# Optimization experiments

Hardware: AMD Instinct MI355X
Metric: run time of the kernel (lower is better)

## Reference

```python
import jax, jax.numpy as jnp
import numpy as np

N = 1048576   # total nodes across batch
B = 128       # number of graphs
H = 128       # hidden_size
NEG_SLOPE = 0.01  # LeakyReLU default


def setup_inputs() -> dict:
    key = jax.random.key(0)
    k1, k2, k3, k4 = jax.random.split(key, 4)
    h = jax.random.normal(k1, (N, H), dtype=jnp.float32)
    attention_query = jax.random.normal(k2, (B, H), dtype=jnp.float32)
    w = jax.random.normal(k3, (2 * H,), dtype=jnp.float32) * (1.0 / np.sqrt(2 * H))
    segment_ids = jnp.sort(jax.random.randint(k4, (N,), 0, B, dtype=jnp.int32))
    return {"h": h, "attention_query": attention_query, "w": w, "segment_ids": segment_ids}


def reference(h, attention_query, w, segment_ids):
    # gate_nn(concat([h, q_rep])) = h @ w[:H] + q[seg] @ w[H:], then LeakyReLU
    w_h, w_q = w[:H], w[H:]
    q_score = attention_query @ w_q                      # [B]
    gate = h @ w_h + q_score[segment_ids]                # [N]
    gate = jnp.where(gate >= 0, gate, NEG_SLOPE * gate)  # LeakyReLU
    # segment softmax over nodes of each graph
    m = jax.ops.segment_max(gate, segment_ids, num_segments=B)   # [B]
    m = jnp.where(jnp.isfinite(m), m, 0.0)               # guard empty segments
    e = jnp.exp(gate - m[segment_ids])                   # [N]
    denom = jax.ops.segment_sum(e, segment_ids, num_segments=B)  # [B]
    alpha = e / jnp.maximum(denom, 1e-20)[segment_ids]   # [N]
    # feat_nn takes first half of concat => just h; weighted segment sum
    pooled = jax.ops.segment_sum(alpha[:, None] * h, segment_ids, num_segments=B)  # [B, H]
    return pooled
```

## Files before the change

### kernel.cpp

```cpp
#include <hip/hip_runtime.h>
#include <math.h>

#define N_ROWS 1048576
#define H 128
#define B 128
#define NEG_SLOPE 0.01f

#define GRID_MAIN 2048
#define ROWS_PB (N_ROWS / GRID_MAIN)
#define ITERS (ROWS_PB / 16)
#define MAXP 256

__global__ __launch_bounds__(256) void qs_init_kernel(const float* __restrict__ aq,
                                                      const float* __restrict__ w,
                                                      float* __restrict__ qs,
                                                      int* __restrict__ counter) {
    if (blockIdx.x == 0 && threadIdx.x < B) counter[threadIdx.x] = 0;
    const int lane = threadIdx.x & 63;
    const int wave = threadIdx.x >> 6;
    const int half = lane >> 5;
    const int hl   = lane & 31;
    const int b    = blockIdx.x * 8 + wave * 2 + half;
    float4 w4 = ((const float4*)(w + H))[hl];
    float4 a4 = ((const float4*)(aq + (long)b * H))[hl];
    float d = a4.x * w4.x + a4.y * w4.y + a4.z * w4.z + a4.w * w4.w;
    #pragma unroll
    for (int off = 1; off < 32; off <<= 1) d += __shfl_xor(d, off, 32);
    if (hl == 0) qs[b] = d;
}

__global__ __launch_bounds__(256) void main_kernel(const float* __restrict__ h,
                                                   const int* __restrict__ seg,
                                                   const float* __restrict__ w,
                                                   const float* __restrict__ qs,
                                                   int* __restrict__ counter,
                                                   float* __restrict__ pm,
                                                   float* __restrict__ pd,
                                                   float* __restrict__ pacc) {
    __shared__ float qs_s[B];
    if (threadIdx.x < B) qs_s[threadIdx.x] = qs[threadIdx.x];
    __syncthreads();

    const int lane = threadIdx.x & 63;
    const int wave = threadIdx.x >> 6;
    const int half = lane >> 5;
    const int hl   = lane & 31;
    const int hwid = wave * 2 + half;
    const long r0  = (long)blockIdx.x * ROWS_PB;

    float4 w4 = ((const float4*)w)[hl];

    int    cur   = -1;
    float  m_run = -1e30f;
    float  d_run = 0.0f;
    float4 acc   = {0.0f, 0.0f, 0.0f, 0.0f};

    for (int it = 0; it < ITERS; ++it) {
        long r1 = r0 + hwid + (long)it * 16;
        long r2 = r1 + 8;
        float4 ha = ((const float4*)(h + r1 * H))[hl];
        float4 hb = ((const float4*)(h + r2 * H))[hl];
        int s1 = seg[r1];
        int s2 = seg[r2];

        #pragma unroll
        for (int k = 0; k < 2; ++k) {
            float4 h4 = k ? hb : ha;
            int    s  = k ? s2 : s1;
            float d = h4.x * w4.x + h4.y * w4.y + h4.z * w4.z + h4.w * w4.w;
            #pragma unroll
            for (int off = 1; off < 32; off <<= 1) d += __shfl_xor(d, off, 32);
            float g = d + qs_s[s];
            g = (g >= 0.0f) ? g : NEG_SLOPE * g;

            if (s != cur) {
                if (cur >= 0) {
                    int slot = 0;
                    if (hl == 0) slot = atomicAdd(counter + cur, 1);
                    slot = __shfl(slot, 0, 32);
                    slot = min(slot, MAXP - 1);
                    long base = (long)cur * MAXP + slot;
                    ((float4*)(pacc + base * H))[hl] = acc;
                    if (hl == 0) { pm[base] = m_run; pd[base] = d_run; }
                }
                cur = s;
                m_run = -1e30f;
                d_run = 0.0f;
                acc = make_float4(0.0f, 0.0f, 0.0f, 0.0f);
            }
            float m_new = fmaxf(m_run, g);
            float sc = __expf(m_run - m_new);
            float e  = __expf(g - m_new);
            acc.x = acc.x * sc + e * h4.x;
            acc.y = acc.y * sc + e * h4.y;
            acc.z = acc.z * sc + e * h4.z;
            acc.w = acc.w * sc + e * h4.w;
            d_run = d_run * sc + e;
            m_run = m_new;
        }
    }
    if (cur >= 0) {
        int slot = 0;
        if (hl == 0) slot = atomicAdd(counter + cur, 1);
        slot = __shfl(slot, 0, 32);
        slot = min(slot, MAXP - 1);
        long base = (long)cur * MAXP + slot;
        ((float4*)(pacc + base * H))[hl] = acc;
        if (hl == 0) { pm[base] = m_run; pd[base] = d_run; }
    }
}

__global__ __launch_bounds__(128) void merge_kernel(const int* __restrict__ counter,
                                                    const float* __restrict__ pm,
                                                    const float* __restrict__ pd,
                                                    const float* __restrict__ pacc,
                                                    float* __restrict__ out) {
    const int s = blockIdx.x;
    const int t = threadIdx.x;
    const int c = min(counter[s], MAXP);
    const long sb = (long)s * MAXP;

    float M = -1e30f;
    for (int j = 0; j < c; ++j) M = fmaxf(M, pm[sb + j]);

    float D = 0.0f, a = 0.0f;
    for (int j = 0; j < c; ++j) {
        float sc = __expf(pm[sb + j] - M);
        D += pd[sb + j] * sc;
        a += pacc[(sb + j) * H + t] * sc;
    }
    out[s * H + t] = (c > 0) ? a / fmaxf(D, 1e-20f) : 0.0f;
}

extern "C" void kernel_launch(void* const* d_in, const int* in_sizes, int n_in,
                              void* d_out, int out_size, void* d_ws, size_t ws_size,
                              hipStream_t stream) {
    const float* h   = (const float*)d_in[0];
    const float* aq  = (const float*)d_in[1];
    const float* w   = (const float*)d_in[2];
    const int*   seg = (const int*)d_in[3];
    float* out = (float*)d_out;

    float* ws      = (float*)d_ws;
    float* qs      = ws;
    int*   counter = (int*)(ws + B);
    float* pm      = ws + 2 * B;
    float* pd      = ws + 2 * B + B * MAXP;
    float* pacc    = ws + 2 * B + 2 * B * MAXP;

    qs_init_kernel<<<16, 256, 0, stream>>>(aq, w, qs, counter);
    main_kernel<<<GRID_MAIN, 256, 0, stream>>>(h, seg, w, qs, counter, pm, pd, pacc);
    merge_kernel<<<B, 128, 0, stream>>>(counter, pm, pd, pacc, out);
}
```

Baseline: 764.8 us.

## Add single-segment fast path in main kernel and parallelize merge reductions

Blocks whose row range falls entirely within one segment now take a fast path. It skips per-row segment-id loads and boundary checks, unrolls four rows per iteration with interleaved shuffle reductions, and combines the two half-wave partials in-register. That halves the partial records written and the atomics issued. The merge kernel now computes the max and denominator with parallel wave reductions and caches scale factors in shared memory, instead of each thread looping serially over all partials twice. Blocks that span a segment boundary keep the original generic loop.

```diff
diff --git a/kernel.cpp b/kernel.cpp
--- a/kernel.cpp
+++ b/kernel.cpp
@@ -8,8 +8,11 @@
 
 #define GRID_MAIN 2048
 #define ROWS_PB (N_ROWS / GRID_MAIN)
-#define ITERS (ROWS_PB / 16)
 #define MAXP 256
+
+__device__ __forceinline__ float dot4(float4 a, float4 b) {
+    return a.x * b.x + a.y * b.y + a.z * b.z + a.w * b.w;
+}
 
 __global__ __launch_bounds__(256) void qs_init_kernel(const float* __restrict__ aq,
                                                       const float* __restrict__ w,
@@ -23,7 +26,7 @@
     const int b    = blockIdx.x * 8 + wave * 2 + half;
     float4 w4 = ((const float4*)(w + H))[hl];
     float4 a4 = ((const float4*)(aq + (long)b * H))[hl];
-    float d = a4.x * w4.x + a4.y * w4.y + a4.z * w4.z + a4.w * w4.w;
+    float d = dot4(a4, w4);
     #pragma unroll
     for (int off = 1; off < 32; off <<= 1) d += __shfl_xor(d, off, 32);
     if (hl == 0) qs[b] = d;
@@ -50,63 +53,131 @@
 
     float4 w4 = ((const float4*)w)[hl];
 
-    int    cur   = -1;
-    float  m_run = -1e30f;
-    float  d_run = 0.0f;
-    float4 acc   = {0.0f, 0.0f, 0.0f, 0.0f};
-
-    for (int it = 0; it < ITERS; ++it) {
-        long r1 = r0 + hwid + (long)it * 16;
-        long r2 = r1 + 8;
-        float4 ha = ((const float4*)(h + r1 * H))[hl];
-        float4 hb = ((const float4*)(h + r2 * H))[hl];
-        int s1 = seg[r1];
-        int s2 = seg[r2];
-
-        #pragma unroll
-        for (int k = 0; k < 2; ++k) {
-            float4 h4 = k ? hb : ha;
-            int    s  = k ? s2 : s1;
-            float d = h4.x * w4.x + h4.y * w4.y + h4.z * w4.z + h4.w * w4.w;
+    const int sFirst = seg[r0];
+    const int sLast  = seg[r0 + ROWS_PB - 1];
+
+    if (sFirst == sLast) {
+        const float qsv = qs_s[sFirst];
+        float  m_run = -1e30f;
+        float  d_run = 0.0f;
+        float4 acc   = {0.0f, 0.0f, 0.0f, 0.0f};
+
+        for (int it = 0; it < ROWS_PB / 32; ++it) {
+            long rb = r0 + hwid + (long)it * 32;
+            float4 h0 = ((const float4*)(h + rb * H))[hl];
+            float4 h1 = ((const float4*)(h + (rb + 8)  * H))[hl];
+            float4 h2 = ((const float4*)(h + (rb + 16) * H))[hl];
+            float4 h3 = ((const float4*)(h + (rb + 24) * H))[hl];
+
+            float d0 = dot4(h0, w4), d1 = dot4(h1, w4);
+            float d2 = dot4(h2, w4), d3 = dot4(h3, w4);
             #pragma unroll
-            for (int off = 1; off < 32; off <<= 1) d += __shfl_xor(d, off, 32);
-            float g = d + qs_s[s];
-            g = (g >= 0.0f) ? g : NEG_SLOPE * g;
-
-            if (s != cur) {
-                if (cur >= 0) {
-                    int slot = 0;
-                    if (hl == 0) slot = atomicAdd(counter + cur, 1);
-                    slot = __shfl(slot, 0, 32);
-                    slot = min(slot, MAXP - 1);
-                    long base = (long)cur * MAXP + slot;
-                    ((float4*)(pacc + base * H))[hl] = acc;
-                    if (hl == 0) { pm[base] = m_run; pd[base] = d_run; }
+            for (int off = 1; off < 32; off <<= 1) {
+                d0 += __shfl_xor(d0, off, 32);
+                d1 += __shfl_xor(d1, off, 32);
+                d2 += __shfl_xor(d2, off, 32);
+                d3 += __shfl_xor(d3, off, 32);
+            }
+            float g0 = d0 + qsv; g0 = (g0 >= 0.0f) ? g0 : NEG_SLOPE * g0;
+            float g1 = d1 + qsv; g1 = (g1 >= 0.0f) ? g1 : NEG_SLOPE * g1;
+            float g2 = d2 + qsv; g2 = (g2 >= 0.0f) ? g2 : NEG_SLOPE * g2;
+            float g3 = d3 + qsv; g3 = (g3 >= 0.0f) ? g3 : NEG_SLOPE * g3;
+
+            #pragma unroll
+            for (int u = 0; u < 4; ++u) {
+                float  g  = (u == 0) ? g0 : (u == 1) ? g1 : (u == 2) ? g2 : g3;
+                float4 hv = (u == 0) ? h0 : (u == 1) ? h1 : (u == 2) ? h2 : h3;
+                float mn = fmaxf(m_run, g);
+                float sc = __expf(m_run - mn);
+                float e  = __expf(g - mn);
+                acc.x = acc.x * sc + e * hv.x;
+                acc.y = acc.y * sc + e * hv.y;
+                acc.z = acc.z * sc + e * hv.z;
+                acc.w = acc.w * sc + e * hv.w;
+                d_run = d_run * sc + e;
+                m_run = mn;
+            }
+        }
+        float m_o = __shfl_xor(m_run, 32);
+        float d_o = __shfl_xor(d_run, 32);
+        float4 a_o;
+        a_o.x = __shfl_xor(acc.x, 32);
+        a_o.y = __shfl_xor(acc.y, 32);
+        a_o.z = __shfl_xor(acc.z, 32);
+        a_o.w = __shfl_xor(acc.w, 32);
+        float M  = fmaxf(m_run, m_o);
+        float ss = __expf(m_run - M);
+        float so = __expf(m_o  - M);
+        float4 am;
+        am.x = acc.x * ss + a_o.x * so;
+        am.y = acc.y * ss + a_o.y * so;
+        am.z = acc.z * ss + a_o.z * so;
+        am.w = acc.w * ss + a_o.w * so;
+        float Dm = d_run * ss + d_o * so;
+
+        int slot = 0;
+        if (lane == 0) slot = atomicAdd(counter + sFirst, 1);
+        slot = min(__shfl(slot, 0), MAXP - 1);
+        long base = (long)sFirst * MAXP + slot;
+        if (half == 0) ((float4*)(pacc + base * H))[hl] = am;
+        if (lane == 0) { pm[base] = M; pd[base] = Dm; }
+    } else {
+        int    cur   = -1;
+        float  m_run = -1e30f;
+        float  d_run = 0.0f;
+        float4 acc   = {0.0f, 0.0f, 0.0f, 0.0f};
+
+        for (int it = 0; it < ROWS_PB / 16; ++it) {
+            long r1 = r0 + hwid + (long)it * 16;
+            long r2 = r1 + 8;
+            float4 ha = ((const float4*)(h + r1 * H))[hl];
+            float4 hb = ((const float4*)(h + r2 * H))[hl];
+            int s1 = seg[r1];
+            int s2 = seg[r2];
+
+            #pragma unroll
+            for (int k = 0; k < 2; ++k) {
+                float4 h4 = k ? hb : ha;
+                int    s  = k ? s2 : s1;
+                float d = dot4(h4, w4);
+                #pragma unroll
+                for (int off = 1; off < 32; off <<= 1) d += __shfl_xor(d, off, 32);
+                float g = d + qs_s[s];
+                g = (g >= 0.0f) ? g : NEG_SLOPE * g;
+
+                if (s != cur) {
+                    if (cur >= 0) {
+                        int slot = 0;
+                        if (hl == 0) slot = atomicAdd(counter + cur, 1);
+                        slot = min(__shfl(slot, 0, 32), MAXP - 1);
+                        long base = (long)cur * MAXP + slot;
+                        ((float4*)(pacc + base * H))[hl] = acc;
+                        if (hl == 0) { pm[base] = m_run; pd[base] = d_run; }
+                    }
+                    cur = s;
+                    m_run = -1e30f;
+                    d_run = 0.0f;
+                    acc = make_float4(0.0f, 0.0f, 0.0f, 0.0f);
                 }
-                cur = s;
-                m_run = -1e30f;
-                d_run = 0.0f;
-                acc = make_float4(0.0f, 0.0f, 0.0f, 0.0f);
+                float mn = fmaxf(m_run, g);
+                float sc = __expf(m_run - mn);
+                float e  = __expf(g - mn);
+                acc.x = acc.x * sc + e * h4.x;
+                acc.y = acc.y * sc + e * h4.y;
+                acc.z = acc.z * sc + e * h4.z;
+                acc.w = acc.w * sc + e * h4.w;
+                d_run = d_run * sc + e;
+                m_run = mn;
             }
-            float m_new = fmaxf(m_run, g);
-            float sc = __expf(m_run - m_new);
-            float e  = __expf(g - m_new);
-            acc.x = acc.x * sc + e * h4.x;
-            acc.y = acc.y * sc + e * h4.y;
-            acc.z = acc.z * sc + e * h4.z;
-            acc.w = acc.w * sc + e * h4.w;
-            d_run = d_run * sc + e;
-            m_run = m_new;
         }
-    }
-    if (cur >= 0) {
-        int slot = 0;
-        if (hl == 0) slot = atomicAdd(counter + cur, 1);
-        slot = __shfl(slot, 0, 32);
-        slot = min(slot, MAXP - 1);
-        long base = (long)cur * MAXP + slot;
-        ((float4*)(pacc + base * H))[hl] = acc;
-        if (hl == 0) { pm[base] = m_run; pd[base] = d_run; }
+        if (cur >= 0) {
+            int slot = 0;
+            if (hl == 0) slot = atomicAdd(counter + cur, 1);
+            slot = min(__shfl(slot, 0, 32), MAXP - 1);
+            long base = (long)cur * MAXP + slot;
+            ((float4*)(pacc + base * H))[hl] = acc;
+            if (hl == 0) { pm[base] = m_run; pd[base] = d_run; }
+        }
     }
 }
 
@@ -120,15 +191,34 @@
     const int c = min(counter[s], MAXP);
     const long sb = (long)s * MAXP;
 
-    float M = -1e30f;
-    for (int j = 0; j < c; ++j) M = fmaxf(M, pm[sb + j]);
-
-    float D = 0.0f, a = 0.0f;
-    for (int j = 0; j < c; ++j) {
+    __shared__ float red[2];
+    __shared__ float scv[MAXP];
+
+    float lm = -1e30f;
+    for (int j = t; j < c; j += 128) lm = fmaxf(lm, pm[sb + j]);
+    #pragma unroll
+    for (int off = 1; off < 64; off <<= 1) lm = fmaxf(lm, __shfl_xor(lm, off));
+    if ((t & 63) == 0) red[t >> 6] = lm;
+    __syncthreads();
+    float M = fmaxf(red[0], red[1]);
+    __syncthreads();
+
+    float ld = 0.0f;
+    for (int j = t; j < c; j += 128) {
         float sc = __expf(pm[sb + j] - M);
-        D += pd[sb + j] * sc;
-        a += pacc[(sb + j) * H + t] * sc;
+        scv[j] = sc;
+        ld += pd[sb + j] * sc;
     }
+    #pragma unroll
+    for (int off = 1; off < 64; off <<= 1) ld += __shfl_xor(ld, off);
+    if ((t & 63) == 0) red[t >> 6] = ld;
+    __syncthreads();
+    float D = red[0] + red[1];
+
+    float a = 0.0f;
+    #pragma unroll 4
+    for (int j = 0; j < c; ++j) a += pacc[(sb + j) * H + t] * scv[j];
+
     out[s * H + t] = (c > 0) ? a / fmaxf(D, 1e-20f) : 0.0f;
 }
 
```

Measured after the change: 703.0 us. -8.1%, faster.
